# Kernel optimization log

Hardware: AMD Instinct MI355X
Metric: run time of the kernel (lower is better)

Reference implementation:

```python
import jax, jax.numpy as jnp
import numpy as np

B, L, C_IN = 16, 512, 32
D_MODEL, D_STATE, D_CONV, EXPAND, PRED_LEN = 128, 16, 4, 2, 96
D_INNER = EXPAND * D_MODEL          # 256
DT_RANK = (D_MODEL + 15) // 16      # 8 (ceil(d_model/16), mamba_ssm default)


def setup_inputs() -> dict:
    key = jax.random.key(0)
    ks = jax.random.split(key, 14)
    f32 = jnp.float32
    nrm = lambda k, shape, sc: jax.random.normal(k, shape, f32) * sc
    inp = {
        "x": jax.random.normal(ks[0], (B, L, C_IN), f32),
        # input_proj: Linear(enc_in, d_model)
        "W_in": nrm(ks[1], (C_IN, D_MODEL), C_IN ** -0.5),
        "b_in": jnp.zeros((D_MODEL,), f32),
        # Mamba in_proj: Linear(d_model, 2*d_inner, bias=False)
        "W_inproj": nrm(ks[2], (D_MODEL, 2 * D_INNER), D_MODEL ** -0.5),
        # depthwise causal conv1d (d_inner, d_conv) + bias
        "conv_w": nrm(ks[3], (D_INNER, D_CONV), D_CONV ** -0.5),
        "conv_b": jnp.zeros((D_INNER,), f32),
        # x_proj: Linear(d_inner, dt_rank + 2*d_state, bias=False)
        "W_xproj": nrm(ks[4], (D_INNER, DT_RANK + 2 * D_STATE), D_INNER ** -0.5),
        # dt_proj: Linear(dt_rank, d_inner) with bias init so softplus(bias) ~ 1e-3..1e-1
        "W_dt": nrm(ks[5], (DT_RANK, D_INNER), DT_RANK ** -0.5),
        "b_dt": jax.random.uniform(ks[6], (D_INNER,), f32, minval=-6.0, maxval=-3.0),
        # S4D-real A init: A = -exp(A_log), A_log = log(1..d_state)
        "A_log": jnp.log(jnp.tile(jnp.arange(1, D_STATE + 1, dtype=f32), (D_INNER, 1))),
        "D": jnp.ones((D_INNER,), f32),
        # Mamba out_proj: Linear(d_inner, d_model, bias=False)
        "W_out": nrm(ks[7], (D_INNER, D_MODEL), D_INNER ** -0.5),
        # output_proj: Linear(d_model*seq_len, pred_len*enc_in)
        "W_outproj": nrm(ks[8], (D_MODEL * L, PRED_LEN * C_IN), (D_MODEL * L) ** -0.5),
        "b_outproj": jnp.zeros((PRED_LEN * C_IN,), f32),
    }
    return inp


def _mamba_forward(x, W_in, b_in, W_inproj, conv_w, conv_b, W_xproj,
                   W_dt, b_dt, A_log, D, W_out, W_outproj, b_outproj):
    Bb, Ll, Cc = x.shape
    d_inner, d_conv = conv_w.shape
    d_state = A_log.shape[1]
    dt_rank = W_dt.shape[0]

    h = x @ W_in + b_in                                  # (B,L,d_model)
    xz = h @ W_inproj                                    # (B,L,2*d_inner)
    u, z = jnp.split(xz, 2, axis=-1)                     # each (B,L,d_inner)

    # causal depthwise conv1d along L
    uc = jnp.transpose(u, (0, 2, 1))                     # (B,d_inner,L)
    kern = conv_w[:, None, :]                            # (d_inner,1,d_conv)
    uc = jax.lax.conv_general_dilated(
        uc, kern, window_strides=(1,), padding=[(d_conv - 1, 0)],
        dimension_numbers=("NCH", "OIH", "NCH"), feature_group_count=d_inner)
    u = jax.nn.silu(jnp.transpose(uc, (0, 2, 1)) + conv_b)   # (B,L,d_inner)

    # input-dependent dt, B, C
    xdbc = u @ W_xproj                                   # (B,L,dt_rank+2*d_state)
    dt = jax.nn.softplus(xdbc[..., :dt_rank] @ W_dt + b_dt)  # (B,L,d_inner)
    Bm = xdbc[..., dt_rank:dt_rank + d_state]            # (B,L,d_state)
    Cm = xdbc[..., dt_rank + d_state:]                   # (B,L,d_state)

    A = -jnp.exp(A_log)                                  # (d_inner,d_state)
    dA = jnp.exp(jnp.einsum('bld,dn->bldn', dt, A))      # discretized A
    dBu = jnp.einsum('bld,bln,bld->bldn', dt, Bm, u)     # discretized B*u

    def step(hstate, inputs):
        dA_t, dBu_t, C_t = inputs                        # (B,d,n),(B,d,n),(B,n)
        hstate = dA_t * hstate + dBu_t
        y_t = jnp.einsum('bdn,bn->bd', hstate, C_t)
        return hstate, y_t

    h0 = jnp.zeros((Bb, d_inner, d_state), u.dtype)
    _, ys = jax.lax.scan(step, h0, (jnp.moveaxis(dA, 1, 0),
                                    jnp.moveaxis(dBu, 1, 0),
                                    jnp.moveaxis(Cm, 1, 0)))
    y = jnp.moveaxis(ys, 0, 1) + u * D                   # (B,L,d_inner)
    y = y * jax.nn.silu(z)                               # gating
    m_out = y @ W_out                                    # (B,L,d_model)

    flat = m_out.reshape(Bb, -1)                         # (B, L*d_model)
    pred = flat @ W_outproj + b_outproj                  # (B, pred_len*enc_in)
    return pred.reshape(Bb, W_outproj.shape[1] // Cc, Cc)


def reference(x, W_in, b_in, W_inproj, conv_w, conv_b, W_xproj,
              W_dt, b_dt, A_log, D, W_out, W_outproj, b_outproj):
    return _mamba_forward(x, W_in, b_in, W_inproj, conv_w, conv_b, W_xproj,
                          W_dt, b_dt, A_log, D, W_out, W_outproj, b_outproj)
```

## Files before the change

kernel.cpp:

```cpp
#include <hip/hip_runtime.h>
#include <math.h>

#define NB 16
#define LL 512
#define CIN 32
#define DM 128
#define DS 16
#define DI 256
#define DTR 8
#define NCOL 3072
#define KTOT 65536
#define ROWS 8192
#define CH 64
#define CLEN 8
#define KC 512
#define KS 128
#define OUTSZ 49152

typedef float f32x2 __attribute__((ext_vector_type(2)));

__device__ __forceinline__ float sigmoidf_(float x){ return 1.f/(1.f+expf(-x)); }
__device__ __forceinline__ float softplusf_(float x){ return (x > 20.f) ? x : log1pf(expf(x)); }

__global__ void __launch_bounds__(256) k_A(
    const float* __restrict__ x, const float* __restrict__ W_in,
    const float* __restrict__ b_in, const float* __restrict__ W_ip,
    const float* __restrict__ cw, const float* __restrict__ cb,
    float* __restrict__ u, float* __restrict__ z) {
  __shared__ float xs[11][32];
  __shared__ float hs[11][128];
  __shared__ float up[11][256];
  int t = threadIdx.x;
  int b  = blockIdx.x >> 6;
  int lt = blockIdx.x & 63;
  int l0 = lt * 8;
  for (int i=t; i<11*32; i+=256) {
    int r = i >> 5, c = i & 31;
    int li = l0 - 3 + r;
    xs[r][c] = (li >= 0) ? x[((b<<9)+li)*CIN + c] : 0.f;
  }
  __syncthreads();
  for (int i=t; i<11*128; i+=256) {
    int r = i >> 7, c = i & 127;
    float acc = b_in[c];
    #pragma unroll
    for (int k=0;k<CIN;k++) acc = fmaf(xs[r][k], W_in[k*DM+c], acc);
    hs[r][c] = acc;
  }
  __syncthreads();
  {
    int c0 = (t & 63)*4;
    int r0 = (t >> 6)*3;
    bool has2 = (r0+2 < 11);
    float acc[3][4] = {};
    for (int k4=0;k4<32;k4++) {
      float4 h0v = *(const float4*)&hs[r0][k4*4];
      float4 h1v = *(const float4*)&hs[r0+1][k4*4];
      float4 h2v = has2 ? *(const float4*)&hs[r0+2][k4*4] : make_float4(0.f,0.f,0.f,0.f);
      float h0a[4]={h0v.x,h0v.y,h0v.z,h0v.w};
      float h1a[4]={h1v.x,h1v.y,h1v.z,h1v.w};
      float h2a[4]={h2v.x,h2v.y,h2v.z,h2v.w};
      #pragma unroll
      for (int j=0;j<4;j++) {
        float4 w = *(const float4*)(W_ip + (k4*4+j)*512 + c0);
        acc[0][0]=fmaf(h0a[j],w.x,acc[0][0]); acc[0][1]=fmaf(h0a[j],w.y,acc[0][1]);
        acc[0][2]=fmaf(h0a[j],w.z,acc[0][2]); acc[0][3]=fmaf(h0a[j],w.w,acc[0][3]);
        acc[1][0]=fmaf(h1a[j],w.x,acc[1][0]); acc[1][1]=fmaf(h1a[j],w.y,acc[1][1]);
        acc[1][2]=fmaf(h1a[j],w.z,acc[1][2]); acc[1][3]=fmaf(h1a[j],w.w,acc[1][3]);
        acc[2][0]=fmaf(h2a[j],w.x,acc[2][0]); acc[2][1]=fmaf(h2a[j],w.y,acc[2][1]);
        acc[2][2]=fmaf(h2a[j],w.z,acc[2][2]); acc[2][3]=fmaf(h2a[j],w.w,acc[2][3]);
      }
    }
    *(float4*)&up[r0  ][c0] = make_float4(acc[0][0],acc[0][1],acc[0][2],acc[0][3]);
    *(float4*)&up[r0+1][c0] = make_float4(acc[1][0],acc[1][1],acc[1][2],acc[1][3]);
    if (has2)
      *(float4*)&up[r0+2][c0] = make_float4(acc[2][0],acc[2][1],acc[2][2],acc[2][3]);
  }
  {
    int c0 = (t & 63)*4;
    int r0 = (t >> 6)*2;
    float acc[2][4] = {};
    for (int k4=0;k4<32;k4++) {
      float4 h0v = *(const float4*)&hs[3+r0][k4*4];
      float4 h1v = *(const float4*)&hs[3+r0+1][k4*4];
      float h0a[4]={h0v.x,h0v.y,h0v.z,h0v.w};
      float h1a[4]={h1v.x,h1v.y,h1v.z,h1v.w};
      #pragma unroll
      for (int j=0;j<4;j++) {
        float4 w = *(const float4*)(W_ip + (k4*4+j)*512 + 256 + c0);
        acc[0][0]=fmaf(h0a[j],w.x,acc[0][0]); acc[0][1]=fmaf(h0a[j],w.y,acc[0][1]);
        acc[0][2]=fmaf(h0a[j],w.z,acc[0][2]); acc[0][3]=fmaf(h0a[j],w.w,acc[0][3]);
        acc[1][0]=fmaf(h1a[j],w.x,acc[1][0]); acc[1][1]=fmaf(h1a[j],w.y,acc[1][1]);
        acc[1][2]=fmaf(h1a[j],w.z,acc[1][2]); acc[1][3]=fmaf(h1a[j],w.w,acc[1][3]);
      }
    }
    #pragma unroll
    for (int i=0;i<2;i++) {
      int gr = (b<<9) + l0 + r0 + i;
      *(float4*)(z + gr*DI + c0) =
        make_float4(acc[i][0],acc[i][1],acc[i][2],acc[i][3]);
    }
  }
  __syncthreads();
  for (int i=t; i<8*256; i+=256) {
    int r = i >> 8, d = i & 255;
    float s = cb[d];
    #pragma unroll
    for (int j=0;j<4;j++) {
      int li = l0 + r - 3 + j;
      if (li >= 0) s = fmaf(cw[d*4+j], up[r+j][d], s);
    }
    int gr = (b<<9) + l0 + r;
    u[gr*DI + d] = s * sigmoidf_(s);
  }
}

__global__ void __launch_bounds__(256) k_xproj(
    const float* __restrict__ u, const float* __restrict__ W_xp,
    float* __restrict__ xdbc) {
  __shared__ float Wt[40][260];
  int t = threadIdx.x;
  for (int i=t; i<256*40; i+=256) {
    int k = i / 40, c = i - k*40;
    Wt[c][k] = W_xp[i];
  }
  __syncthreads();
  int idx = blockIdx.x*256 + t;
  int r = idx / 40, c = idx - r*40;
  const float4* ur4 = (const float4*)(u + r*DI);
  const float4* wc4 = (const float4*)&Wt[c][0];
  float acc = 0.f;
  #pragma unroll 8
  for (int k4=0;k4<64;k4++) {
    float4 uv = ur4[k4];
    float4 wv = wc4[k4];
    acc = fmaf(uv.x, wv.x, acc);
    acc = fmaf(uv.y, wv.y, acc);
    acc = fmaf(uv.z, wv.z, acc);
    acc = fmaf(uv.w, wv.w, acc);
  }
  xdbc[idx] = acc;
}

__global__ void __launch_bounds__(256) k_scan1(
    const float* __restrict__ u, const float* __restrict__ xdbc,
    const float* __restrict__ Wdt, const float* __restrict__ bdt,
    const float* __restrict__ A_log,
    float* __restrict__ Hc, float* __restrict__ Sdt) {
  __shared__ float xl[CLEN][40];
  int t = threadIdx.x;
  int b = blockIdx.x >> 6, c = blockIdx.x & 63, d = t;
  int l0 = c * CLEN;
  int row0 = (b<<9) + l0;
  for (int i=t; i<CLEN*40; i+=256) xl[i/40][i%40] = xdbc[row0*40 + i];
  __syncthreads();
  float A[16], hsv[16];
  #pragma unroll
  for (int n=0;n<16;n++){ A[n] = -expf(A_log[d*16+n]); hsv[n]=0.f; }
  float wdt[DTR];
  #pragma unroll
  for (int j=0;j<DTR;j++) wdt[j] = Wdt[j*DI+d];
  float bdtv = bdt[d];
  float sdt = 0.f;
  for (int l=0;l<CLEN;++l) {
    float acc = bdtv;
    #pragma unroll
    for (int j=0;j<DTR;j++) acc = fmaf(xl[l][j], wdt[j], acc);
    float dtv = softplusf_(acc);
    sdt += dtv;
    float du = dtv * u[((row0+l)<<8) + d];
    #pragma unroll
    for (int n=0;n<16;n++) {
      float a = expf(dtv*A[n]);
      hsv[n] = fmaf(a, hsv[n], du * xl[l][DTR+n]);
    }
  }
  int hbase = ((b*CH + c)*DS)*DI + d;
  #pragma unroll
  for (int n=0;n<16;n++) Hc[hbase + n*DI] = hsv[n];
  Sdt[(b*CH + c)*DI + d] = sdt;
}

__global__ void k_scan2(const float* __restrict__ A_log, const float* __restrict__ Hc,
                        const float* __restrict__ Sdt, float* __restrict__ Hst) {
  int d = threadIdx.x;
  int b = blockIdx.x >> 4, n = blockIdx.x & 15;
  float A = -expf(A_log[d*16+n]);
  float hs = 0.f;
  for (int c=0;c<CH;c++) {
    int off = ((b*CH + c)*DS + n)*DI + d;
    Hst[off] = hs;
    float sdt = Sdt[(b*CH + c)*DI + d];
    hs = fmaf(expf(A*sdt), hs, Hc[off]);
  }
}

__global__ void __launch_bounds__(256) k_scan3(
    const float* __restrict__ u, const float* __restrict__ z,
    const float* __restrict__ xdbc, const float* __restrict__ Wdt,
    const float* __restrict__ bdt, const float* __restrict__ A_log,
    const float* __restrict__ Dp, const float* __restrict__ Hst,
    const float* __restrict__ W_out, float* __restrict__ mo) {
  __shared__ float ym[CLEN][256];
  __shared__ float xl[CLEN][40];
  int t = threadIdx.x;
  int b = blockIdx.x >> 6, c = blockIdx.x & 63, d = t;
  int l0 = c * CLEN;
  int row0 = (b<<9) + l0;
  for (int i=t; i<CLEN*40; i+=256) xl[i/40][i%40] = xdbc[row0*40 + i];
  __syncthreads();
  int hbase = ((b*CH + c)*DS)*DI + d;
  float A[16], hsv[16];
  #pragma unroll
  for (int n=0;n<16;n++){ A[n] = -expf(A_log[d*16+n]); hsv[n] = Hst[hbase + n*DI]; }
  float wdt[DTR];
  #pragma unroll
  for (int j=0;j<DTR;j++) wdt[j] = Wdt[j*DI+d];
  float bdtv = bdt[d];
  float Dv = Dp[d];
  for (int l=0;l<CLEN;++l) {
    int row = row0 + l;
    float acc = bdtv;
    #pragma unroll
    for (int j=0;j<DTR;j++) acc = fmaf(xl[l][j], wdt[j], acc);
    float dtv = softplusf_(acc);
    float uv = u[(row<<8) + d];
    float zv = z[(row<<8) + d];
    float du = dtv * uv;
    float y = 0.f;
    #pragma unroll
    for (int n=0;n<16;n++) {
      float a = expf(dtv*A[n]);
      hsv[n] = fmaf(a, hsv[n], du * xl[l][DTR+n]);
      y = fmaf(hsv[n], xl[l][DTR+DS+n], y);
    }
    y = fmaf(uv, Dv, y);
    ym[l][d] = y * (zv * sigmoidf_(zv));
  }
  __syncthreads();
  int cc = t & 127;
  int rg = (t >> 7) * 4;
  float acc[4] = {};
  for (int k4=0;k4<64;k4++) {
    float w0 = W_out[(k4*4+0)*DM+cc];
    float w1 = W_out[(k4*4+1)*DM+cc];
    float w2 = W_out[(k4*4+2)*DM+cc];
    float w3 = W_out[(k4*4+3)*DM+cc];
    #pragma unroll
    for (int o=0;o<4;o++) {
      float4 yv = *(const float4*)&ym[rg+o][k4*4];
      acc[o] = fmaf(yv.w, w3, fmaf(yv.z, w2, fmaf(yv.y, w1, fmaf(yv.x, w0, acc[o]))));
    }
  }
  #pragma unroll
  for (int o=0;o<4;o++) mo[(row0+rg+o)*DM + cc] = acc[o];
}

__global__ void __launch_bounds__(256) k_final(
    const float* __restrict__ flat, const float* __restrict__ W,
    float* __restrict__ part) {
  __shared__ float lds[KC][16];
  int t = threadIdx.x;
  int n0 = blockIdx.x * 512;
  int k0 = blockIdx.y * KC;
  for (int i = t; i < 16*(KC/4); i += 256) {
    int bb  = i & 15;
    int kk4 = i >> 4;
    float4 v = *(const float4*)(flat + bb*KTOT + k0 + kk4*4);
    lds[kk4*4+0][bb] = v.x; lds[kk4*4+1][bb] = v.y;
    lds[kk4*4+2][bb] = v.z; lds[kk4*4+3][bb] = v.w;
  }
  __syncthreads();
  int c0 = n0 + t*2;
  float2 acc[16];
  #pragma unroll
  for (int b=0;b<16;b++) acc[b] = make_float2(0.f,0.f);
  const float* Wp = W + (size_t)k0*NCOL + c0;
  for (int kk=0; kk<KC; kk+=4) {
    f32x2 w0 = __builtin_nontemporal_load((const f32x2*)(Wp + (size_t)(kk+0)*NCOL));
    f32x2 w1 = __builtin_nontemporal_load((const f32x2*)(Wp + (size_t)(kk+1)*NCOL));
    f32x2 w2 = __builtin_nontemporal_load((const f32x2*)(Wp + (size_t)(kk+2)*NCOL));
    f32x2 w3 = __builtin_nontemporal_load((const f32x2*)(Wp + (size_t)(kk+3)*NCOL));
    const float4* f0 = (const float4*)&lds[kk+0][0];
    const float4* f1 = (const float4*)&lds[kk+1][0];
    const float4* f2 = (const float4*)&lds[kk+2][0];
    const float4* f3 = (const float4*)&lds[kk+3][0];
    #pragma unroll
    for (int q=0;q<4;q++) {
      float4 fa = f0[q], fb = f1[q], fc = f2[q], fd = f3[q];
      float fs0[4] = {fa.x,fa.y,fa.z,fa.w};
      float fs1[4] = {fb.x,fb.y,fb.z,fb.w};
      float fs2[4] = {fc.x,fc.y,fc.z,fc.w};
      float fs3[4] = {fd.x,fd.y,fd.z,fd.w};
      #pragma unroll
      for (int j=0;j<4;j++) {
        int b = q*4+j;
        acc[b].x=fmaf(fs0[j],w0.x,acc[b].x); acc[b].y=fmaf(fs0[j],w0.y,acc[b].y);
        acc[b].x=fmaf(fs1[j],w1.x,acc[b].x); acc[b].y=fmaf(fs1[j],w1.y,acc[b].y);
        acc[b].x=fmaf(fs2[j],w2.x,acc[b].x); acc[b].y=fmaf(fs2[j],w2.y,acc[b].y);
        acc[b].x=fmaf(fs3[j],w3.x,acc[b].x); acc[b].y=fmaf(fs3[j],w3.y,acc[b].y);
      }
    }
  }
  float* p = part + (size_t)blockIdx.y*OUTSZ;
  #pragma unroll
  for (int b=0;b<16;b++) {
    f32x2 v; v.x = acc[b].x; v.y = acc[b].y;
    __builtin_nontemporal_store(v, (f32x2*)(p + b*NCOL + c0));
  }
}

__global__ void k_reduce(const float* __restrict__ part, const float* __restrict__ bias,
                         float* __restrict__ out) {
  int idx = blockIdx.x*256 + threadIdx.x;
  float acc = bias[idx % NCOL];
  #pragma unroll 8
  for (int s=0;s<KS;s++)
    acc += __builtin_nontemporal_load(part + (size_t)s*OUTSZ + idx);
  out[idx] = acc;
}

extern "C" void kernel_launch(void* const* d_in, const int* in_sizes, int n_in,
                              void* d_out, int out_size, void* d_ws, size_t ws_size,
                              hipStream_t stream) {
  const float* x        = (const float*)d_in[0];
  const float* W_in     = (const float*)d_in[1];
  const float* b_in     = (const float*)d_in[2];
  const float* W_inproj = (const float*)d_in[3];
  const float* conv_w   = (const float*)d_in[4];
  const float* conv_b   = (const float*)d_in[5];
  const float* W_xproj  = (const float*)d_in[6];
  const float* W_dt     = (const float*)d_in[7];
  const float* b_dt     = (const float*)d_in[8];
  const float* A_log    = (const float*)d_in[9];
  const float* Dp       = (const float*)d_in[10];
  const float* W_out    = (const float*)d_in[11];
  const float* W_outproj= (const float*)d_in[12];
  const float* b_outproj= (const float*)d_in[13];
  float* out = (float*)d_out;
  float* ws  = (float*)d_ws;

  float* u    = ws;
  float* z    = ws + 2097152;
  float* xdbc = ws + 4194304;
  float* Hc   = ws + 4521984;
  float* Sdt  = ws + 8716288;
  float* Hst  = ws + 8978432;
  float* mo   = ws + 13172736;
  float* part = ws + 14221312;

  k_A     <<<1024, 256, 0, stream>>>(x, W_in, b_in, W_inproj, conv_w, conv_b, u, z);
  k_xproj <<<1280, 256, 0, stream>>>(u, W_xproj, xdbc);
  k_scan1 <<<1024, 256, 0, stream>>>(u, xdbc, W_dt, b_dt, A_log, Hc, Sdt);
  k_scan2 <<<256,  256, 0, stream>>>(A_log, Hc, Sdt, Hst);
  k_scan3 <<<1024, 256, 0, stream>>>(u, z, xdbc, W_dt, b_dt, A_log, Dp, Hst, W_out, mo);
  k_final <<<dim3(6, KS), 256, 0, stream>>>(mo, W_outproj, part);
  k_reduce<<<192,  256, 0, stream>>>(part, b_outproj, out);
}
```

Baseline: 285.3 us.

## Fuse input projection, conv, x_proj and chunk scan into one kernel

Merges the projection/conv kernel, the x_proj kernel and the first chunk-scan kernel into a single kernel per (batch, 8-step chunk) tile, keeping u and xdbc in shared memory for the later stages. This removes two kernel launches and the global re-reads of u and xdbc between stages. The x_proj now reads W_xproj directly from global memory in each block instead of from a transposed shared copy, and x_proj work is spread unevenly (320 outputs over 256 threads). Larger shared-memory use may lower occupancy.

```diff
diff --git a/kernel.cpp b/kernel.cpp
--- a/kernel.cpp
+++ b/kernel.cpp
@@ -22,18 +22,24 @@
 __device__ __forceinline__ float sigmoidf_(float x){ return 1.f/(1.f+expf(-x)); }
 __device__ __forceinline__ float softplusf_(float x){ return (x > 20.f) ? x : log1pf(expf(x)); }
 
-__global__ void __launch_bounds__(256) k_A(
+__global__ void __launch_bounds__(256) k_mega1(
     const float* __restrict__ x, const float* __restrict__ W_in,
     const float* __restrict__ b_in, const float* __restrict__ W_ip,
     const float* __restrict__ cw, const float* __restrict__ cb,
-    float* __restrict__ u, float* __restrict__ z) {
+    const float* __restrict__ W_xp, const float* __restrict__ Wdt,
+    const float* __restrict__ bdt, const float* __restrict__ A_log,
+    float* __restrict__ u, float* __restrict__ z,
+    float* __restrict__ xdbc, float* __restrict__ Hc, float* __restrict__ Sdt) {
   __shared__ float xs[11][32];
   __shared__ float hs[11][128];
   __shared__ float up[11][256];
+  __shared__ float ul[CLEN][256];
+  __shared__ float xl[CLEN][40];
   int t = threadIdx.x;
   int b  = blockIdx.x >> 6;
   int lt = blockIdx.x & 63;
   int l0 = lt * 8;
+  int row0 = (b<<9) + l0;
   for (int i=t; i<11*32; i+=256) {
     int r = i >> 5, c = i & 31;
     int li = l0 - 3 + r;
@@ -96,7 +102,7 @@
     }
     #pragma unroll
     for (int i=0;i<2;i++) {
-      int gr = (b<<9) + l0 + r0 + i;
+      int gr = row0 + r0 + i;
       *(float4*)(z + gr*DI + c0) =
         make_float4(acc[i][0],acc[i][1],acc[i][2],acc[i][3]);
     }
@@ -110,75 +116,54 @@
       int li = l0 + r - 3 + j;
       if (li >= 0) s = fmaf(cw[d*4+j], up[r+j][d], s);
     }
-    int gr = (b<<9) + l0 + r;
-    u[gr*DI + d] = s * sigmoidf_(s);
-  }
-}
-
-__global__ void __launch_bounds__(256) k_xproj(
-    const float* __restrict__ u, const float* __restrict__ W_xp,
-    float* __restrict__ xdbc) {
-  __shared__ float Wt[40][260];
-  int t = threadIdx.x;
-  for (int i=t; i<256*40; i+=256) {
-    int k = i / 40, c = i - k*40;
-    Wt[c][k] = W_xp[i];
-  }
-  __syncthreads();
-  int idx = blockIdx.x*256 + t;
-  int r = idx / 40, c = idx - r*40;
-  const float4* ur4 = (const float4*)(u + r*DI);
-  const float4* wc4 = (const float4*)&Wt[c][0];
-  float acc = 0.f;
-  #pragma unroll 8
-  for (int k4=0;k4<64;k4++) {
-    float4 uv = ur4[k4];
-    float4 wv = wc4[k4];
-    acc = fmaf(uv.x, wv.x, acc);
-    acc = fmaf(uv.y, wv.y, acc);
-    acc = fmaf(uv.z, wv.z, acc);
-    acc = fmaf(uv.w, wv.w, acc);
-  }
-  xdbc[idx] = acc;
-}
-
-__global__ void __launch_bounds__(256) k_scan1(
-    const float* __restrict__ u, const float* __restrict__ xdbc,
-    const float* __restrict__ Wdt, const float* __restrict__ bdt,
-    const float* __restrict__ A_log,
-    float* __restrict__ Hc, float* __restrict__ Sdt) {
-  __shared__ float xl[CLEN][40];
-  int t = threadIdx.x;
-  int b = blockIdx.x >> 6, c = blockIdx.x & 63, d = t;
-  int l0 = c * CLEN;
-  int row0 = (b<<9) + l0;
-  for (int i=t; i<CLEN*40; i+=256) xl[i/40][i%40] = xdbc[row0*40 + i];
-  __syncthreads();
-  float A[16], hsv[16];
-  #pragma unroll
-  for (int n=0;n<16;n++){ A[n] = -expf(A_log[d*16+n]); hsv[n]=0.f; }
-  float wdt[DTR];
-  #pragma unroll
-  for (int j=0;j<DTR;j++) wdt[j] = Wdt[j*DI+d];
-  float bdtv = bdt[d];
-  float sdt = 0.f;
-  for (int l=0;l<CLEN;++l) {
-    float acc = bdtv;
-    #pragma unroll
-    for (int j=0;j<DTR;j++) acc = fmaf(xl[l][j], wdt[j], acc);
-    float dtv = softplusf_(acc);
-    sdt += dtv;
-    float du = dtv * u[((row0+l)<<8) + d];
-    #pragma unroll
-    for (int n=0;n<16;n++) {
-      float a = expf(dtv*A[n]);
-      hsv[n] = fmaf(a, hsv[n], du * xl[l][DTR+n]);
-    }
-  }
-  int hbase = ((b*CH + c)*DS)*DI + d;
-  #pragma unroll
-  for (int n=0;n<16;n++) Hc[hbase + n*DI] = hsv[n];
-  Sdt[(b*CH + c)*DI + d] = sdt;
+    float uv = s * sigmoidf_(s);
+    ul[r][d] = uv;
+    u[(row0+r)*DI + d] = uv;
+  }
+  __syncthreads();
+  for (int i=t; i<CLEN*40; i+=256) {
+    int r = i / 40, cc = i - r*40;
+    float acc = 0.f;
+    #pragma unroll 8
+    for (int k4=0;k4<64;k4++) {
+      float4 uv = *(const float4*)&ul[r][k4*4];
+      acc = fmaf(uv.x, W_xp[(k4*4+0)*40+cc], acc);
+      acc = fmaf(uv.y, W_xp[(k4*4+1)*40+cc], acc);
+      acc = fmaf(uv.z, W_xp[(k4*4+2)*40+cc], acc);
+      acc = fmaf(uv.w, W_xp[(k4*4+3)*40+cc], acc);
+    }
+    xl[r][cc] = acc;
+    xdbc[row0*40 + i] = acc;
+  }
+  __syncthreads();
+  {
+    int d = t, c = lt;
+    float A[16], hsv[16];
+    #pragma unroll
+    for (int n=0;n<16;n++){ A[n] = -expf(A_log[d*16+n]); hsv[n]=0.f; }
+    float wdt[DTR];
+    #pragma unroll
+    for (int j=0;j<DTR;j++) wdt[j] = Wdt[j*DI+d];
+    float bdtv = bdt[d];
+    float sdt = 0.f;
+    for (int l=0;l<CLEN;++l) {
+      float acc = bdtv;
+      #pragma unroll
+      for (int j=0;j<DTR;j++) acc = fmaf(xl[l][j], wdt[j], acc);
+      float dtv = softplusf_(acc);
+      sdt += dtv;
+      float du = dtv * ul[l][d];
+      #pragma unroll
+      for (int n=0;n<16;n++) {
+        float a = expf(dtv*A[n]);
+        hsv[n] = fmaf(a, hsv[n], du * xl[l][DTR+n]);
+      }
+    }
+    int hbase = ((b*CH + c)*DS)*DI + d;
+    #pragma unroll
+    for (int n=0;n<16;n++) Hc[hbase + n*DI] = hsv[n];
+    Sdt[(b*CH + c)*DI + d] = sdt;
+  }
 }
 
 __global__ void k_scan2(const float* __restrict__ A_log, const float* __restrict__ Hc,
@@ -349,9 +334,9 @@
   float* mo   = ws + 13172736;
   float* part = ws + 14221312;
 
-  k_A     <<<1024, 256, 0, stream>>>(x, W_in, b_in, W_inproj, conv_w, conv_b, u, z);
-  k_xproj <<<1280, 256, 0, stream>>>(u, W_xproj, xdbc);
-  k_scan1 <<<1024, 256, 0, stream>>>(u, xdbc, W_dt, b_dt, A_log, Hc, Sdt);
+  k_mega1 <<<1024, 256, 0, stream>>>(x, W_in, b_in, W_inproj, conv_w, conv_b,
+                                     W_xproj, W_dt, b_dt, A_log,
+                                     u, z, xdbc, Hc, Sdt);
   k_scan2 <<<256,  256, 0, stream>>>(A_log, Hc, Sdt, Hst);
   k_scan3 <<<1024, 256, 0, stream>>>(u, z, xdbc, W_dt, b_dt, A_log, Dp, Hst, W_out, mo);
   k_final <<<dim3(6, KS), 256, 0, stream>>>(mo, W_outproj, part);
```

After: 274.1 us. 3.9% less time.
